# Kernel optimization log

Hardware: AMD Instinct MI355X
Metric: run time of the kernel (lower is better)

The kernel has to match this reference:

```python
import jax, jax.numpy as jnp
import numpy as np

N_NODES = 100000


def _gcn_conv(x, edge_index, W, b, n):
    """PyG GCNConv: h = x @ W; add self-loops; symmetric deg^-1/2 norm; scatter-add; + b."""
    h = x @ W                                            # [N, F_out]
    src = jnp.concatenate([edge_index[0], jnp.arange(n)])  # self-loops appended
    dst = jnp.concatenate([edge_index[1], jnp.arange(n)])
    deg = jax.ops.segment_sum(jnp.ones_like(dst, dtype=h.dtype), dst, num_segments=n)
    dinv = jnp.where(deg > 0, jax.lax.rsqrt(deg), 0.0)   # deg^-1/2 with inf->0
    norm = dinv[src] * dinv[dst]                         # [E+N]
    msg = h[src] * norm[:, None]                         # gather + scale
    out = jax.ops.segment_sum(msg, dst, num_segments=n)  # scatter-add
    return out + b


def setup_inputs() -> dict:
    key = jax.random.key(0)
    ks = jax.random.split(key, 4)
    x = jax.random.normal(ks[0], (N_NODES, 128), dtype=jnp.float32)
    edge_index = jax.random.randint(ks[1], (2, 1600000), 0, N_NODES, dtype=jnp.int64)
    W1 = jax.random.normal(ks[2], (128, 128), dtype=jnp.float32) * (1.0 / np.sqrt(128))
    b1 = jnp.zeros((128,), dtype=jnp.float32)
    W2 = jax.random.normal(ks[3], (128, 16), dtype=jnp.float32) * (1.0 / np.sqrt(128))
    b2 = jnp.zeros((16,), dtype=jnp.float32)
    return {"x": x, "edge_index": edge_index, "W1": W1, "b1": b1, "W2": W2, "b2": b2}


def reference(x, edge_index, W1, b1, W2, b2):
    n = x.shape[0]
    h = jax.nn.relu(_gcn_conv(x, edge_index, W1, b1, n))
    out = _gcn_conv(h, edge_index, W2, b2, n)
    return out
```

## Files before the change

kernel.cpp:

```cpp
#include <hip/hip_runtime.h>
#include <hip/hip_bf16.h>

typedef __attribute__((ext_vector_type(8))) short bf16x8;
typedef __attribute__((ext_vector_type(4))) float f32x4;

#define ELL_W 64
#define BSH   8
#define BCAP  4608
#define CHUNK 4096


__device__ __forceinline__ float bf2f(unsigned short u) {
    return __uint_as_float(((unsigned int)u) << 16);
}
__device__ __forceinline__ unsigned short f2bf(float f) {
    unsigned int u = __float_as_uint(f);
    unsigned int r = (u + 0x7fffu + ((u >> 16) & 1u)) >> 16;
    return (unsigned short)r;
}

__global__ void zero_kernel(int* __restrict__ a, int n) {
    int i = blockIdx.x * blockDim.x + threadIdx.x;
    if (i < n) a[i] = 0;
}


__global__ __launch_bounds__(256) void p1_partition_kernel(const int* __restrict__ ei, int E, int N, int NB,
                                                           int* __restrict__ gcur, int* __restrict__ bucket) {
    __shared__ int hist[512];
    __shared__ int gbase[512];
    __shared__ int cur2[512];
    int tid = threadIdx.x;
    int c0 = blockIdx.x * CHUNK;

    for (int i = tid; i < NB; i += 256) { hist[i] = 0; cur2[i] = 0; }
    __syncthreads();

    int rec[16], bkt[16];
#pragma unroll
    for (int k = 0; k < 16; ++k) {
        int e = c0 + k * 256 + tid;
        int b = -1, r = 0;
        if (e < E) {
            int s = ei[e], d = ei[E + e];
            if ((unsigned)s < (unsigned)N && (unsigned)d < (unsigned)N) {
                b = d >> BSH;
                r = (s << BSH) | (d & ((1 << BSH) - 1));
            }
        }
        bkt[k] = b; rec[k] = r;
        if (b >= 0) atomicAdd(&hist[b], 1);
    }
    __syncthreads();

    for (int i = tid; i < NB; i += 256) {
        int c = hist[i];
        gbase[i] = (c > 0) ? atomicAdd(&gcur[i * 16], c) : 0;
    }
    __syncthreads();

#pragma unroll
    for (int k = 0; k < 16; ++k) {
        int b = bkt[k];
        if (b >= 0) {
            int r = atomicAdd(&cur2[b], 1);
            int pos = gbase[b] + r;
            if (pos < BCAP) bucket[(size_t)b * BCAP + pos] = rec[k];
        }
    }
}


__global__ __launch_bounds__(256) void p2_ell_kernel(const int* __restrict__ bucket,
                                                     const int* __restrict__ gcur, int N,
                                                     int* __restrict__ cursor, int* __restrict__ ell) {
    int b = blockIdx.x;
    int cnt = gcur[b * 16]; if (cnt > BCAP) cnt = BCAP;
    const int* reg = &bucket[(size_t)b * BCAP];
    for (int k = threadIdx.x; k < cnt; k += 256) {
        int rec = reg[k];
        int s = (int)(((unsigned)rec) >> BSH);
        int dst = (b << BSH) | (rec & ((1 << BSH) - 1));
        if (dst < N) {
            int pos = atomicAdd(&cursor[dst], 1);
            if (pos < ELL_W) ell[(size_t)dst * ELL_W + pos] = s;
        }
    }
}

__global__ void compute_dinv_kernel(const int* __restrict__ deg, float* __restrict__ dinv, int N) {
    int i = blockIdx.x * blockDim.x + threadIdx.x;
    if (i < N) dinv[i] = rsqrtf((float)(deg[i] + 1));
}


__global__ void build_wfrag_kernel(const float* __restrict__ W1, unsigned short* __restrict__ wfrag) {
    int t = blockIdx.x * blockDim.x + threadIdx.x;
    if (t >= 2048) return;
    int ln = t & 63;
    int blk = t >> 6;
    int j = blk >> 2, k0 = blk & 3;
    int nn = ln & 15, cc = ln >> 4;
    int n = j * 16 + nn;
    unsigned short tmp[8];
#pragma unroll
    for (int i = 0; i < 8; ++i) {
        int k = k0 * 32 + cc * 8 + i;
        tmp[i] = f2bf(W1[(size_t)k * 128 + n]);
    }
    *(uint4*)&wfrag[(size_t)t * 8] = *(const uint4*)tmp;
}


__global__ __launch_bounds__(256) void gemm1_mfma_kernel(const float* __restrict__ X,
                                                         const unsigned short* __restrict__ wfrag,
                                                         unsigned short* __restrict__ H, int N) {
    __shared__ __align__(16) unsigned short wl[16384];
    int tid = threadIdx.x;
    {
        uint4* dst = (uint4*)wl;
        const uint4* src = (const uint4*)wfrag;
        for (int idx = tid; idx < 2048; idx += 256) dst[idx] = src[idx];
    }
    __syncthreads();

    int lane = tid & 63;
    int wave = tid >> 6;
    int m0 = blockIdx.x * 128 + wave * 32;
    int mrow = lane & 15;
    int kc = lane >> 4;

    f32x4 acc[2][8];
#pragma unroll
    for (int rt = 0; rt < 2; ++rt)
#pragma unroll
        for (int j = 0; j < 8; ++j) acc[rt][j] = (f32x4)(0.f);

#pragma unroll
    for (int k0 = 0; k0 < 4; ++k0) {
        bf16x8 a[2];
#pragma unroll
        for (int rt = 0; rt < 2; ++rt) {
            int row = m0 + rt * 16 + mrow;
            bf16x8 av = (bf16x8)(short)0;
            if (row < N) {
                const float4* p = (const float4*)&X[(size_t)row * 128 + k0 * 32 + kc * 8];
                float4 v0 = p[0], v1 = p[1];
                av[0] = (short)f2bf(v0.x); av[1] = (short)f2bf(v0.y);
                av[2] = (short)f2bf(v0.z); av[3] = (short)f2bf(v0.w);
                av[4] = (short)f2bf(v1.x); av[5] = (short)f2bf(v1.y);
                av[6] = (short)f2bf(v1.z); av[7] = (short)f2bf(v1.w);
            }
            a[rt] = av;
        }
#pragma unroll
        for (int j = 0; j < 8; ++j) {
            bf16x8 b = *(const bf16x8*)&wl[((size_t)(j * 4 + k0) * 64 + lane) * 8];
            acc[0][j] = __builtin_amdgcn_mfma_f32_16x16x32_bf16(a[0], b, acc[0][j], 0, 0, 0);
            acc[1][j] = __builtin_amdgcn_mfma_f32_16x16x32_bf16(a[1], b, acc[1][j], 0, 0, 0);
        }
    }

#pragma unroll
    for (int rt = 0; rt < 2; ++rt) {
#pragma unroll
        for (int r = 0; r < 4; ++r) {
            int row = m0 + rt * 16 + 4 * kc + r;
            if (row < N) {
#pragma unroll
                for (int j = 0; j < 8; ++j) {
                    H[(size_t)row * 128 + j * 16 + mrow] = f2bf(acc[rt][j][r]);
                }
            }
        }
    }
}


__global__ __launch_bounds__(256) void agg128_fused_kernel(const unsigned short* __restrict__ H,
                                                           const int* __restrict__ ell,
                                                           const int* __restrict__ deg,
                                                           const float* __restrict__ dinv,
                                                           const float* __restrict__ b1,
                                                           const float* __restrict__ W2,
                                                           unsigned short* __restrict__ h2out, int N) {
    __shared__ float gbuf[4][128];
    int lane = threadIdx.x & 63;
    int w = threadIdx.x >> 6;
    int i = blockIdx.x * 4 + w;
    if (i >= N) return;

    int n = lane & 15;
    int q = lane >> 4;

    float w2r[32];
#pragma unroll
    for (int m = 0; m < 32; ++m) {
        int mm = (m + 8 * q) & 31;
        w2r[m] = W2[(size_t)(q * 32 + mm) * 16 + n];
    }

    int d = deg[i]; if (d > ELL_W) d = ELL_W;
    float di = dinv[i];

    ushort2 hv = *(const ushort2*)&H[(size_t)i * 128 + 2 * lane];
    float ax = di * bf2f(hv.x);
    float ay = di * bf2f(hv.y);

    const int* row = &ell[(size_t)i * ELL_W];
#pragma unroll 4
    for (int e = 0; e < d; ++e) {
        int s = row[e];
        float wt = dinv[s];
        ushort2 h2 = *(const ushort2*)&H[(size_t)s * 128 + 2 * lane];
        ax += wt * bf2f(h2.x);
        ay += wt * bf2f(h2.y);
    }
    float2 bb = *(const float2*)&b1[2 * lane];
    float gx = fmaxf(di * ax + bb.x, 0.f);
    float gy = fmaxf(di * ay + bb.y, 0.f);

    *(float2*)&gbuf[w][2 * lane] = make_float2(gx, gy);
    asm volatile("s_waitcnt lgkmcnt(0)" ::: "memory");

    float partial = 0.f;
#pragma unroll
    for (int t = 0; t < 8; ++t) {
        int off = (t * 4 + 8 * q) & 31;
        float4 gv = *(const float4*)&gbuf[w][q * 32 + off];
        partial += gv.x * w2r[t * 4 + 0] + gv.y * w2r[t * 4 + 1] +
                   gv.z * w2r[t * 4 + 2] + gv.w * w2r[t * 4 + 3];
    }
    partial += __shfl_xor(partial, 16, 64);
    partial += __shfl_xor(partial, 32, 64);
    if (lane < 16) h2out[(size_t)i * 16 + lane] = f2bf(partial);
}


__global__ __launch_bounds__(256) void agg16_kernel(const unsigned short* __restrict__ H,
                                                    const int* __restrict__ ell,
                                                    const int* __restrict__ deg,
                                                    const float* __restrict__ dinv,
                                                    const float* __restrict__ b2,
                                                    float* __restrict__ out, int N) {
    int lane = threadIdx.x & 63;
    int i = blockIdx.x * 4 + (threadIdx.x >> 6);
    if (i >= N) return;
    int t = lane & 15;
    int q = lane >> 4;

    int d = deg[i]; if (d > ELL_W) d = ELL_W;
    float di = dinv[i];
    const int* row = &ell[(size_t)i * ELL_W];

    float partial = (q == 0) ? di * bf2f(H[(size_t)i * 16 + t]) : 0.f;
#pragma unroll 2
    for (int e = q; e < d; e += 4) {
        int s = row[e];
        float wt = dinv[s];
        partial += wt * bf2f(H[(size_t)s * 16 + t]);
    }
    partial += __shfl_xor(partial, 16, 64);
    partial += __shfl_xor(partial, 32, 64);
    if (lane < 16) out[(size_t)i * 16 + t] = di * partial + b2[t];
}


extern "C" void kernel_launch(void* const* d_in, const int* in_sizes, int n_in,
                              void* d_out, int out_size, void* d_ws, size_t ws_size,
                              hipStream_t stream) {
    const float* x = (const float*)d_in[0];
    const int* ei = (const int*)d_in[1];
    const float* W1 = (const float*)d_in[2];
    const float* b1 = (const float*)d_in[3];
    const float* W2 = (const float*)d_in[4];
    const float* b2 = (const float*)d_in[5];
    float* out = (float*)d_out;

    const int N = in_sizes[0] / 128;
    const int E = in_sizes[1] / 2;
    const int NB = (N + (1 << BSH) - 1) >> BSH;

    char* base = (char*)d_ws;
    size_t off = 0;
    auto align_up = [](size_t v) { return (v + 255) & ~(size_t)255; };

    int* cursor = (int*)(base + off);                      off = align_up(off + (size_t)N * 4);
    float* dinv = (float*)(base + off);                    off = align_up(off + (size_t)N * 4);
    int* ell = (int*)(base + off);                         off = align_up(off + (size_t)N * ELL_W * 4);
    int* gcur = (int*)(base + off);                        off = align_up(off + (size_t)NB * 16 * 4);
    int* bucket = (int*)(base + off);                      off = align_up(off + (size_t)NB * BCAP * 4);
    unsigned short* wfrag = (unsigned short*)(base + off); off = align_up(off + (size_t)16384 * 2);
    unsigned short* h1 = (unsigned short*)(base + off);    off = align_up(off + (size_t)N * 128 * 2);
    unsigned short* h2 = (unsigned short*)(base + off);    off = align_up(off + (size_t)N * 16 * 2);

    zero_kernel<<<(N + 255) / 256, 256, 0, stream>>>(cursor, N);
    zero_kernel<<<(NB * 16 + 255) / 256, 256, 0, stream>>>(gcur, NB * 16);
    build_wfrag_kernel<<<8, 256, 0, stream>>>(W1, wfrag);

    int nchunks = (E + CHUNK - 1) / CHUNK;
    p1_partition_kernel<<<nchunks, 256, 0, stream>>>(ei, E, N, NB, gcur, bucket);
    p2_ell_kernel<<<NB, 256, 0, stream>>>(bucket, gcur, N, cursor, ell);
    compute_dinv_kernel<<<(N + 255) / 256, 256, 0, stream>>>(cursor, dinv, N);

    gemm1_mfma_kernel<<<(N + 127) / 128, 256, 0, stream>>>(x, wfrag, h1, N);
    agg128_fused_kernel<<<(N + 3) / 4, 256, 0, stream>>>(h1, ell, cursor, dinv, b1, W2, h2, N);
    agg16_kernel<<<(N + 3) / 4, 256, 0, stream>>>(h2, ell, cursor, dinv, b2, out, N);
}
```

Measured before the change: 231.4 us.

## Prescale features by source dinv and batch ELL neighbor gathers

Folds the source-side deg^-1/2 factor into the producers: the GEMM1 epilogue scales each row of H by dinv, and the fused agg128 kernel scales its projected output by dinv before storing. Both aggregation kernels then sum raw neighbor rows and no longer do a dependent dinv[s] gather per edge. The agg128 loop also loads ELL indices as int4 and issues eight independent row gathers per iteration into two accumulators, adding memory-level parallelism. Prescaling before bf16 rounding changes rounding slightly and costs a few more registers.

```diff
diff --git a/kernel.cpp b/kernel.cpp
--- a/kernel.cpp
+++ b/kernel.cpp
@@ -114,6 +114,7 @@
 
 __global__ __launch_bounds__(256) void gemm1_mfma_kernel(const float* __restrict__ X,
                                                          const unsigned short* __restrict__ wfrag,
+                                                         const float* __restrict__ dinv,
                                                          unsigned short* __restrict__ H, int N) {
     __shared__ __align__(16) unsigned short wl[16384];
     int tid = threadIdx.x;
@@ -167,9 +168,10 @@
         for (int r = 0; r < 4; ++r) {
             int row = m0 + rt * 16 + 4 * kc + r;
             if (row < N) {
+                float dv = dinv[row];
 #pragma unroll
                 for (int j = 0; j < 8; ++j) {
-                    H[(size_t)row * 128 + j * 16 + mrow] = f2bf(acc[rt][j][r]);
+                    H[(size_t)row * 128 + j * 16 + mrow] = f2bf(dv * acc[rt][j][r]);
                 }
             }
         }
@@ -204,18 +206,38 @@
     float di = dinv[i];
 
     ushort2 hv = *(const ushort2*)&H[(size_t)i * 128 + 2 * lane];
-    float ax = di * bf2f(hv.x);
-    float ay = di * bf2f(hv.y);
+    float ax = bf2f(hv.x), ay = bf2f(hv.y);
+    float bx = 0.f, by = 0.f;
 
     const int* row = &ell[(size_t)i * ELL_W];
-#pragma unroll 4
-    for (int e = 0; e < d; ++e) {
+    int e = 0;
+    for (; e + 8 <= d; e += 8) {
+        int4 sA = *(const int4*)&row[e];
+        int4 sB = *(const int4*)&row[e + 4];
+        ushort2 g0 = *(const ushort2*)&H[(size_t)sA.x * 128 + 2 * lane];
+        ushort2 g1 = *(const ushort2*)&H[(size_t)sA.y * 128 + 2 * lane];
+        ushort2 g2 = *(const ushort2*)&H[(size_t)sA.z * 128 + 2 * lane];
+        ushort2 g3 = *(const ushort2*)&H[(size_t)sA.w * 128 + 2 * lane];
+        ushort2 g4 = *(const ushort2*)&H[(size_t)sB.x * 128 + 2 * lane];
+        ushort2 g5 = *(const ushort2*)&H[(size_t)sB.y * 128 + 2 * lane];
+        ushort2 g6 = *(const ushort2*)&H[(size_t)sB.z * 128 + 2 * lane];
+        ushort2 g7 = *(const ushort2*)&H[(size_t)sB.w * 128 + 2 * lane];
+        ax += bf2f(g0.x); ay += bf2f(g0.y);
+        bx += bf2f(g1.x); by += bf2f(g1.y);
+        ax += bf2f(g2.x); ay += bf2f(g2.y);
+        bx += bf2f(g3.x); by += bf2f(g3.y);
+        ax += bf2f(g4.x); ay += bf2f(g4.y);
+        bx += bf2f(g5.x); by += bf2f(g5.y);
+        ax += bf2f(g6.x); ay += bf2f(g6.y);
+        bx += bf2f(g7.x); by += bf2f(g7.y);
+    }
+    for (; e < d; ++e) {
         int s = row[e];
-        float wt = dinv[s];
-        ushort2 h2 = *(const ushort2*)&H[(size_t)s * 128 + 2 * lane];
-        ax += wt * bf2f(h2.x);
-        ay += wt * bf2f(h2.y);
-    }
+        ushort2 g = *(const ushort2*)&H[(size_t)s * 128 + 2 * lane];
+        ax += bf2f(g.x); ay += bf2f(g.y);
+    }
+    ax += bx; ay += by;
+
     float2 bb = *(const float2*)&b1[2 * lane];
     float gx = fmaxf(di * ax + bb.x, 0.f);
     float gy = fmaxf(di * ay + bb.y, 0.f);
@@ -233,7 +255,7 @@
     }
     partial += __shfl_xor(partial, 16, 64);
     partial += __shfl_xor(partial, 32, 64);
-    if (lane < 16) h2out[(size_t)i * 16 + lane] = f2bf(partial);
+    if (lane < 16) h2out[(size_t)i * 16 + lane] = f2bf(di * partial);
 }
 
 
@@ -253,12 +275,11 @@
     float di = dinv[i];
     const int* row = &ell[(size_t)i * ELL_W];
 
-    float partial = (q == 0) ? di * bf2f(H[(size_t)i * 16 + t]) : 0.f;
+    float partial = (q == 0) ? bf2f(H[(size_t)i * 16 + t]) : 0.f;
 #pragma unroll 2
     for (int e = q; e < d; e += 4) {
         int s = row[e];
-        float wt = dinv[s];
-        partial += wt * bf2f(H[(size_t)s * 16 + t]);
+        partial += bf2f(H[(size_t)s * 16 + t]);
     }
     partial += __shfl_xor(partial, 16, 64);
     partial += __shfl_xor(partial, 32, 64);
@@ -303,7 +324,7 @@
     p2_ell_kernel<<<NB, 256, 0, stream>>>(bucket, gcur, N, cursor, ell);
     compute_dinv_kernel<<<(N + 255) / 256, 256, 0, stream>>>(cursor, dinv, N);
 
-    gemm1_mfma_kernel<<<(N + 127) / 128, 256, 0, stream>>>(x, wfrag, h1, N);
+    gemm1_mfma_kernel<<<(N + 127) / 128, 256, 0, stream>>>(x, wfrag, dinv, h1, N);
     agg128_fused_kernel<<<(N + 3) / 4, 256, 0, stream>>>(h1, ell, cursor, dinv, b1, W2, h2, N);
     agg16_kernel<<<(N + 3) / 4, 256, 0, stream>>>(h2, ell, cursor, dinv, b2, out, N);
 }
```

Result: no change. 228.4 us (-1.3%).

## Pre-scale features by source dinv and split neighbor gathers across half-waves

Applied to the files above, without the earlier changes.

Folds the source-side deg^-1/2 factor into the GEMM epilogue and the layer-2 projection output, so both aggregation kernels no longer gather dinv[s] per edge. The 128-wide aggregation now has each half-wave process alternate neighbors with 8-byte loads, reads four ELL indices at a time, and combines the halves with a shuffle. Each wave now handles four nodes and the block count drops accordingly. A new pad kernel fills ELL rows up to a multiple of four with a dummy index pointing at an extra zeroed row of H. This removes the per-edge dinv gathers and loop-tail handling, at the cost of one extra launch and redundant zero-row gathers.

```diff
diff --git a/kernel.cpp b/kernel.cpp
--- a/kernel.cpp
+++ b/kernel.cpp
@@ -88,6 +88,18 @@
     }
 }
 
+
+__global__ void pad_kernel(const int* __restrict__ deg, int N,
+                           int* __restrict__ ell, unsigned short* __restrict__ h1) {
+    int i = blockIdx.x * blockDim.x + threadIdx.x;
+    if (i < 128) h1[(size_t)N * 128 + i] = 0;
+    if (i < N) {
+        int d = deg[i]; if (d > ELL_W) d = ELL_W;
+        int d4 = (d + 3) & ~3; if (d4 > ELL_W) d4 = ELL_W;
+        for (int k = d; k < d4; ++k) ell[(size_t)i * ELL_W + k] = N;
+    }
+}
+
 __global__ void compute_dinv_kernel(const int* __restrict__ deg, float* __restrict__ dinv, int N) {
     int i = blockIdx.x * blockDim.x + threadIdx.x;
     if (i < N) dinv[i] = rsqrtf((float)(deg[i] + 1));
@@ -114,6 +126,7 @@
 
 __global__ __launch_bounds__(256) void gemm1_mfma_kernel(const float* __restrict__ X,
                                                          const unsigned short* __restrict__ wfrag,
+                                                         const float* __restrict__ dinv,
                                                          unsigned short* __restrict__ H, int N) {
     __shared__ __align__(16) unsigned short wl[16384];
     int tid = threadIdx.x;
@@ -167,9 +180,10 @@
         for (int r = 0; r < 4; ++r) {
             int row = m0 + rt * 16 + 4 * kc + r;
             if (row < N) {
+                float dv = dinv[row];
 #pragma unroll
                 for (int j = 0; j < 8; ++j) {
-                    H[(size_t)row * 128 + j * 16 + mrow] = f2bf(acc[rt][j][r]);
+                    H[(size_t)row * 128 + j * 16 + mrow] = f2bf(dv * acc[rt][j][r]);
                 }
             }
         }
@@ -187,11 +201,12 @@
     __shared__ float gbuf[4][128];
     int lane = threadIdx.x & 63;
     int w = threadIdx.x >> 6;
-    int i = blockIdx.x * 4 + w;
-    if (i >= N) return;
+    int i0 = blockIdx.x * 16 + w * 4;
 
     int n = lane & 15;
     int q = lane >> 4;
+    int sub = lane >> 5;
+    int fl = lane & 31;
 
     float w2r[32];
 #pragma unroll
@@ -200,40 +215,60 @@
         w2r[m] = W2[(size_t)(q * 32 + mm) * 16 + n];
     }
 
-    int d = deg[i]; if (d > ELL_W) d = ELL_W;
-    float di = dinv[i];
-
-    ushort2 hv = *(const ushort2*)&H[(size_t)i * 128 + 2 * lane];
-    float ax = di * bf2f(hv.x);
-    float ay = di * bf2f(hv.y);
-
-    const int* row = &ell[(size_t)i * ELL_W];
-#pragma unroll 4
-    for (int e = 0; e < d; ++e) {
-        int s = row[e];
-        float wt = dinv[s];
-        ushort2 h2 = *(const ushort2*)&H[(size_t)s * 128 + 2 * lane];
-        ax += wt * bf2f(h2.x);
-        ay += wt * bf2f(h2.y);
-    }
-    float2 bb = *(const float2*)&b1[2 * lane];
-    float gx = fmaxf(di * ax + bb.x, 0.f);
-    float gy = fmaxf(di * ay + bb.y, 0.f);
-
-    *(float2*)&gbuf[w][2 * lane] = make_float2(gx, gy);
-    asm volatile("s_waitcnt lgkmcnt(0)" ::: "memory");
-
-    float partial = 0.f;
-#pragma unroll
-    for (int t = 0; t < 8; ++t) {
-        int off = (t * 4 + 8 * q) & 31;
-        float4 gv = *(const float4*)&gbuf[w][q * 32 + off];
-        partial += gv.x * w2r[t * 4 + 0] + gv.y * w2r[t * 4 + 1] +
-                   gv.z * w2r[t * 4 + 2] + gv.w * w2r[t * 4 + 3];
-    }
-    partial += __shfl_xor(partial, 16, 64);
-    partial += __shfl_xor(partial, 32, 64);
-    if (lane < 16) h2out[(size_t)i * 16 + lane] = f2bf(partial);
+    for (int nn = 0; nn < 4; ++nn) {
+        int i = i0 + nn;
+        if (i >= N) break;
+        int d = deg[i]; if (d > ELL_W) d = ELL_W;
+        int d4 = (d + 3) & ~3; if (d4 > ELL_W) d4 = ELL_W;
+        float di = dinv[i];
+
+        ushort4 hv = *(const ushort4*)&H[(size_t)i * 128 + 4 * fl];
+        float a0 = sub ? 0.f : bf2f(hv.x);
+        float a1 = sub ? 0.f : bf2f(hv.y);
+        float a2 = sub ? 0.f : bf2f(hv.z);
+        float a3 = sub ? 0.f : bf2f(hv.w);
+
+        const int* row = &ell[(size_t)i * ELL_W];
+        for (int e = 0; e < d4; e += 4) {
+            int4 sv = *(const int4*)&row[e];
+            int sA = sub ? sv.y : sv.x;
+            int sB = sub ? sv.w : sv.z;
+            ushort4 gA = *(const ushort4*)&H[(size_t)sA * 128 + 4 * fl];
+            ushort4 gB = *(const ushort4*)&H[(size_t)sB * 128 + 4 * fl];
+            a0 += bf2f(gA.x) + bf2f(gB.x);
+            a1 += bf2f(gA.y) + bf2f(gB.y);
+            a2 += bf2f(gA.z) + bf2f(gB.z);
+            a3 += bf2f(gA.w) + bf2f(gB.w);
+        }
+
+        a0 += __shfl_xor(a0, 32, 64);
+        a1 += __shfl_xor(a1, 32, 64);
+        a2 += __shfl_xor(a2, 32, 64);
+        a3 += __shfl_xor(a3, 32, 64);
+
+        if (sub == 0) {
+            float4 bb = *(const float4*)&b1[4 * fl];
+            float4 gv;
+            gv.x = fmaxf(di * a0 + bb.x, 0.f);
+            gv.y = fmaxf(di * a1 + bb.y, 0.f);
+            gv.z = fmaxf(di * a2 + bb.z, 0.f);
+            gv.w = fmaxf(di * a3 + bb.w, 0.f);
+            *(float4*)&gbuf[w][4 * fl] = gv;
+        }
+        asm volatile("s_waitcnt lgkmcnt(0)" ::: "memory");
+
+        float partial = 0.f;
+#pragma unroll
+        for (int t = 0; t < 8; ++t) {
+            int off = (t * 4 + 8 * q) & 31;
+            float4 gv = *(const float4*)&gbuf[w][q * 32 + off];
+            partial += gv.x * w2r[t * 4 + 0] + gv.y * w2r[t * 4 + 1] +
+                       gv.z * w2r[t * 4 + 2] + gv.w * w2r[t * 4 + 3];
+        }
+        partial += __shfl_xor(partial, 16, 64);
+        partial += __shfl_xor(partial, 32, 64);
+        if (lane < 16) h2out[(size_t)i * 16 + lane] = f2bf(di * partial);
+    }
 }
 
 
@@ -253,12 +288,11 @@
     float di = dinv[i];
     const int* row = &ell[(size_t)i * ELL_W];
 
-    float partial = (q == 0) ? di * bf2f(H[(size_t)i * 16 + t]) : 0.f;
+    float partial = (q == 0) ? bf2f(H[(size_t)i * 16 + t]) : 0.f;
 #pragma unroll 2
     for (int e = q; e < d; e += 4) {
         int s = row[e];
-        float wt = dinv[s];
-        partial += wt * bf2f(H[(size_t)s * 16 + t]);
+        partial += bf2f(H[(size_t)s * 16 + t]);
     }
     partial += __shfl_xor(partial, 16, 64);
     partial += __shfl_xor(partial, 32, 64);
@@ -291,7 +325,7 @@
     int* gcur = (int*)(base + off);                        off = align_up(off + (size_t)NB * 16 * 4);
     int* bucket = (int*)(base + off);                      off = align_up(off + (size_t)NB * BCAP * 4);
     unsigned short* wfrag = (unsigned short*)(base + off); off = align_up(off + (size_t)16384 * 2);
-    unsigned short* h1 = (unsigned short*)(base + off);    off = align_up(off + (size_t)N * 128 * 2);
+    unsigned short* h1 = (unsigned short*)(base + off);    off = align_up(off + (size_t)(N + 1) * 128 * 2);
     unsigned short* h2 = (unsigned short*)(base + off);    off = align_up(off + (size_t)N * 16 * 2);
 
     zero_kernel<<<(N + 255) / 256, 256, 0, stream>>>(cursor, N);
@@ -301,9 +335,10 @@
     int nchunks = (E + CHUNK - 1) / CHUNK;
     p1_partition_kernel<<<nchunks, 256, 0, stream>>>(ei, E, N, NB, gcur, bucket);
     p2_ell_kernel<<<NB, 256, 0, stream>>>(bucket, gcur, N, cursor, ell);
+    pad_kernel<<<(N + 255) / 256, 256, 0, stream>>>(cursor, N, ell, h1);
     compute_dinv_kernel<<<(N + 255) / 256, 256, 0, stream>>>(cursor, dinv, N);
 
-    gemm1_mfma_kernel<<<(N + 127) / 128, 256, 0, stream>>>(x, wfrag, h1, N);
-    agg128_fused_kernel<<<(N + 3) / 4, 256, 0, stream>>>(h1, ell, cursor, dinv, b1, W2, h2, N);
+    gemm1_mfma_kernel<<<(N + 127) / 128, 256, 0, stream>>>(x, wfrag, dinv, h1, N);
+    agg128_fused_kernel<<<(N + 15) / 16, 256, 0, stream>>>(h1, ell, cursor, dinv, b1, W2, h2, N);
     agg16_kernel<<<(N + 3) / 4, 256, 0, stream>>>(h2, ell, cursor, dinv, b2, out, N);
 }
```

Measured after the change: 214.5 us. -7.3%, faster.
